# Performance work log

Hardware: AMD Instinct MI355X
Metric: run time of the kernel (lower is better)

## Reference

```python
import jax, jax.numpy as jnp
import numpy as np

D = 64
H = 256


def _directions(d):
    """Taylor-coefficient directions matching Bilaplacian._set_up_taylor_coefficients."""
    eye = np.eye(d, dtype=np.float32)
    dirs1 = 4.0 * eye                                   # (D, D): 4*e_i
    pairs_neq = np.array([(i, j) for i in range(d) for j in range(d) if i != j])
    dirs2 = 3.0 * eye[pairs_neq[:, 0]] + eye[pairs_neq[:, 1]]      # (D(D-1), D): 3 e_i + e_j
    pairs_lt = np.array([(i, j) for i in range(d) for j in range(i + 1, d)])
    dirs3 = 2.0 * eye[pairs_lt[:, 0]] + 2.0 * eye[pairs_lt[:, 1]]  # (D(D-1)/2, D): 2 e_i + 2 e_j
    return jnp.asarray(dirs1), jnp.asarray(dirs2), jnp.asarray(dirs3)


def setup_inputs() -> dict:
    key = jax.random.key(0)
    ks = jax.random.split(key, 7)
    x = jax.random.normal(ks[0], (D,), dtype=jnp.float32)
    W1 = jax.random.normal(ks[1], (H, D), dtype=jnp.float32) / np.sqrt(D)
    b1 = 0.1 * jax.random.normal(ks[2], (H,), dtype=jnp.float32)
    W2 = jax.random.normal(ks[3], (H, H), dtype=jnp.float32) / np.sqrt(H)
    b2 = 0.1 * jax.random.normal(ks[4], (H,), dtype=jnp.float32)
    W3 = jax.random.normal(ks[5], (1, H), dtype=jnp.float32) / np.sqrt(H)
    b3 = 0.1 * jax.random.normal(ks[6], (1,), dtype=jnp.float32)
    return {"x": x, "W1": W1, "b1": b1, "W2": W2, "b2": b2, "W3": W3, "b3": b3}


def _bilaplacian(x, W1, b1, W2, b2, W3, b3):
    d = x.shape[0]

    def f(z):
        h = jnp.tanh(W1 @ z + b1)
        h = jnp.tanh(W2 @ h + b2)
        return W3 @ h + b3  # (1,)

    def d4(v):
        # 4th directional derivative d^4/dt^4 f(x + t v) via Taylor-mode (nested jvp)
        g1 = lambda z: jax.jvp(f, (z,), (v,))[1]
        g2 = lambda z: jax.jvp(g1, (z,), (v,))[1]
        g3 = lambda z: jax.jvp(g2, (z,), (v,))[1]
        return jax.jvp(g3, (x,), (v,))[1]

    dirs1, dirs2, dirs3 = _directions(d)
    S1 = jax.vmap(d4)(dirs1).sum(0)
    S2 = jax.vmap(d4)(dirs2).sum(0)
    S3 = jax.vmap(d4)(dirs3).sum(0)
    # Polarization weights s.t. alpha*S1 + beta*S2 + gamma*S3 = sum_{i,j} d^4 f / dx_i^2 dx_j^2
    alpha = (1.0 + 13.0 * (d - 1) / 9.0) / 256.0
    beta = -1.0 / 36.0
    gamma = 5.0 / 96.0
    return alpha * S1 + beta * S2 + gamma * S3


def reference(x, W1, b1, W2, b2, W3, b3):
    return _bilaplacian(x, W1, b1, W2, b2, W3, b3)
```

## Files before the change

### kernel.cpp

```cpp
#include <hip/hip_runtime.h>
#include <hip/hip_bf16.h>


#define C_F    0
#define H0_F   1024
#define R2_F   1280
#define E_F    1536
#define Q_F    2560
#define S5_F   2816
#define U_F    3072
#define W1T_F  3328
#define G_F    19712
#define P_F    85248

__global__ __launch_bounds__(256) void k1_kernel(
    const float* __restrict__ x, const float* __restrict__ W1,
    const float* __restrict__ b1, float* __restrict__ ws_f,
    double* __restrict__ acc, int* __restrict__ cnt) {
    __shared__ __align__(16) float smem[2 * 64 * 68];
    int tid = threadIdx.x, b = blockIdx.x;

    if (b == 0) {
        float* xs = smem;
        if (tid < 64) xs[tid] = x[tid];
        __syncthreads();
        const float4* row = (const float4*)(W1 + tid * 64);
        const float4* xv4 = (const float4*)xs;
        float u0 = b1[tid], r2v = 0.f;
        #pragma unroll
        for (int k = 0; k < 16; k++) {
            float4 w = row[k], xv = xv4[k];
            u0  += w.x * xv.x + w.y * xv.y + w.z * xv.z + w.w * xv.w;
            r2v += w.x * w.x + w.y * w.y + w.z * w.z + w.w * w.w;
        }
        float T = tanhf(u0), s = 1.f - T * T;
        ws_f[C_F + tid]       = s;
        ws_f[C_F + 256 + tid] = -2.f * T * s;
        ws_f[C_F + 512 + tid] = s * (6.f * T * T - 2.f);
        ws_f[C_F + 768 + tid] = s * T * (16.f - 24.f * T * T);
        ws_f[H0_F + tid] = T;
        ws_f[R2_F + tid] = r2v;
        if (tid == 0) { *acc = 0.0; *cnt = 0; }
    } else if (b <= 16) {
        int tb = b - 1, nb = tb >> 2, pb = tb & 3;
        float* As = smem;
        float* Bs = smem + 64 * 68;
        for (int idx = tid; idx < 4096; idx += 256) {
            int r = idx >> 6, i = idx & 63;
            As[i * 68 + r] = W1[(nb * 64 + r) * 64 + i];
            Bs[i * 68 + r] = W1[(pb * 64 + r) * 64 + i];
        }
        __syncthreads();
        int r0 = (tid & 15) * 4, c0 = (tid >> 4) * 4;
        float a[4][4] = {};
        for (int i = 0; i < 64; i++) {
            float4 av = *(const float4*)&As[i * 68 + r0];
            float4 bv = *(const float4*)&Bs[i * 68 + c0];
            float ar[4] = {av.x, av.y, av.z, av.w};
            float br[4] = {bv.x, bv.y, bv.z, bv.w};
            #pragma unroll
            for (int rr = 0; rr < 4; rr++)
                #pragma unroll
                for (int cc = 0; cc < 4; cc++)
                    a[rr][cc] = fmaf(ar[rr], br[cc], a[rr][cc]);
        }
        float* G = ws_f + G_F;
        #pragma unroll
        for (int rr = 0; rr < 4; rr++)
            #pragma unroll
            for (int cc = 0; cc < 4; cc++)
                G[(nb * 64 + r0 + rr) * 256 + pb * 64 + c0 + cc] = a[rr][cc];
    } else {
        int base = (b - 17) * 4096;
        float* W1t = ws_f + W1T_F;
        for (int idx = base + tid; idx < base + 4096; idx += 256) {
            int n = idx >> 6, i = idx & 63;
            W1t[i * 256 + n] = W1[idx];
        }
    }
}

__global__ __launch_bounds__(256) void k2_kernel(
    const float* __restrict__ W1, const float* __restrict__ W2,
    const float* __restrict__ b2, const float* __restrict__ W3,
    float* __restrict__ ws_f) {
    __shared__ __align__(16) float smem[64 * 34 + 64 * 68];
    int tid = threadIdx.x, b = blockIdx.x;
    const float* c1g = ws_f + C_F;
    const float* c2g = ws_f + C_F + 256;
    const float* c4g = ws_f + C_F + 768;

    if (b < 8) {
        int m0 = b * 32;
        float* Wc = smem;
        float* Bc = smem + 64 * 34;
        float acc2[2][4] = {};
        int tm2 = (tid & 15) * 2, ti = (tid >> 4) * 4;
        for (int nc = 0; nc < 4; nc++) {
            __syncthreads();
            for (int idx = tid; idx < 2048; idx += 256) {
                int mm = idx >> 6, nn = idx & 63;
                Wc[nn * 34 + mm] = W2[(m0 + mm) * 256 + nc * 64 + nn];
            }
            for (int idx = tid; idx < 4096; idx += 256) {
                int nn = idx >> 6, ii = idx & 63, n = nc * 64 + nn;
                Bc[nn * 68 + ii] = c1g[n] * W1[n * 64 + ii];
            }
            __syncthreads();
            for (int nn = 0; nn < 64; nn++) {
                float2 a2 = *(const float2*)&Wc[nn * 34 + tm2];
                float4 b4 = *(const float4*)&Bc[nn * 68 + ti];
                float br[4] = {b4.x, b4.y, b4.z, b4.w};
                #pragma unroll
                for (int j = 0; j < 4; j++) {
                    acc2[0][j] = fmaf(a2.x, br[j], acc2[0][j]);
                    acc2[1][j] = fmaf(a2.y, br[j], acc2[1][j]);
                }
            }
        }
        float* P = ws_f + P_F;
        #pragma unroll
        for (int j = 0; j < 4; j++) {
            P[(m0 + tm2) * 64 + ti + j]     = acc2[0][j];
            P[(m0 + tm2 + 1) * 64 + ti + j] = acc2[1][j];
        }
    } else if (b < 12) {
        int m0 = (b - 8) * 64;
        float* Ws  = smem;
        float* h0s = smem + 64 * 65;
        float* part = h0s + 256;
        h0s[tid] = ws_f[H0_F + tid];
        int mm = tid & 63, nq = tid >> 6;
        float partial = 0.f;
        for (int nc = 0; nc < 4; nc++) {
            __syncthreads();
            for (int idx = tid; idx < 4096; idx += 256) {
                int m2 = idx >> 6, nn = idx & 63;
                Ws[nn * 65 + m2] = W2[(m0 + m2) * 256 + nc * 64 + nn];
            }
            __syncthreads();
            #pragma unroll
            for (int k = 0; k < 16; k++) {
                int nn = nq * 16 + k;
                partial = fmaf(Ws[nn * 65 + mm], h0s[nc * 64 + nn], partial);
            }
        }
        part[nq * 64 + mm] = partial;
        __syncthreads();
        if (tid < 64) {
            int m = m0 + tid;
            float v = b2[m] + part[tid] + part[64 + tid] + part[128 + tid] + part[192 + tid];
            float T2 = tanhf(v), s2 = 1.f - T2 * T2, w3 = W3[m];
            float* E = ws_f + E_F;
            E[m]       = w3 * s2;
            E[256 + m] = -2.f * w3 * T2 * s2;
            E[512 + m] = w3 * s2 * (6.f * T2 * T2 - 2.f);
            E[768 + m] = w3 * s2 * T2 * (16.f - 24.f * T2 * T2);
        }
    } else {
        int m = b - 12;
        float* cw  = smem;
        float* red = smem + 256;
        float w2r = W2[m * 256 + tid], c2r = c2g[tid];
        float cwv = c2r * w2r;
        cw[tid] = cwv;
        __syncthreads();
        const float* G = ws_f + G_F;
        float km = 0.f;
        #pragma unroll 4
        for (int np = 0; np < 256; np++) {
            float g = G[np * 256 + tid];
            km = fmaf(g * g, cw[np], km);
        }
        float r2r = ws_f[R2_F + tid], c4r = c4g[tid];
        float uv  = km * cwv;
        float qv  = cwv * r2r;
        float s5v = w2r * c4r * r2r * r2r;
        for (int o = 32; o > 0; o >>= 1) {
            uv  += __shfl_down(uv, o, 64);
            qv  += __shfl_down(qv, o, 64);
            s5v += __shfl_down(s5v, o, 64);
        }
        int w = tid >> 6;
        if ((tid & 63) == 0) { red[w * 3] = uv; red[w * 3 + 1] = qv; red[w * 3 + 2] = s5v; }
        __syncthreads();
        if (tid == 0) {
            ws_f[U_F + m]  = red[0] + red[3] + red[6] + red[9];
            ws_f[Q_F + m]  = red[1] + red[4] + red[7] + red[10];
            ws_f[S5_F + m] = red[2] + red[5] + red[8] + red[11];
        }
    }
}

__global__ __launch_bounds__(256) void k3_kernel(
    const float* __restrict__ W2, float* __restrict__ ws_f,
    double* __restrict__ acc, int* __restrict__ cnt, float* __restrict__ out) {
    __shared__ __align__(16) float smem[64 + 16];
    int tid = threadIdx.x, m = blockIdx.x;
    float* Ps  = smem;
    float* red = smem + 64;
    const float* P = ws_f + P_F;
    if (tid < 64) Ps[tid] = P[m * 64 + tid];
    __syncthreads();
    const float* W1t = ws_f + W1T_F;
    float T = 0.f;
    #pragma unroll 4
    for (int i = 0; i < 64; i++) T = fmaf(Ps[i], W1t[i * 256 + tid], T);
    float w2r = W2[m * 256 + tid];
    float c2r = ws_f[C_F + 256 + tid], c3r = ws_f[C_F + 512 + tid];
    float r2r = ws_f[R2_F + tid];
    float s3v = c2r * w2r * T * T;
    float s4v = c3r * r2r * w2r * T;
    float p2v = (tid < 64) ? Ps[tid] * Ps[tid] : 0.f;
    for (int o = 32; o > 0; o >>= 1) {
        s3v += __shfl_down(s3v, o, 64);
        s4v += __shfl_down(s4v, o, 64);
        p2v += __shfl_down(p2v, o, 64);
    }
    int w = tid >> 6;
    if ((tid & 63) == 0) { red[w * 3] = s3v; red[w * 3 + 1] = s4v; red[w * 3 + 2] = p2v; }
    __syncthreads();
    if (tid == 0) {
        float s3 = red[0] + red[3] + red[6] + red[9];
        float s4 = red[1] + red[4] + red[7] + red[10];
        float p2 = red[2] + red[5] + red[8] + red[11];
        const float* E = ws_f + E_F;
        float qm = ws_f[Q_F + m], um = ws_f[U_F + m], s5m = ws_f[S5_F + m];
        float y = E[768 + m] * p2 * p2
                + E[512 + m] * (2.f * qm * p2 + 4.f * s3)
                + E[256 + m] * (qm * qm + 2.f * um + 4.f * s4)
                + E[m] * s5m;
        atomicAdd(acc, (double)y);
        __threadfence();
        int t = atomicAdd(cnt, 1);
        if (t == 255) {
            __threadfence();
            out[0] = (float)atomicAdd(acc, 0.0);
        }
    }
}

extern "C" void kernel_launch(void* const* d_in, const int* in_sizes, int n_in,
                              void* d_out, int out_size, void* d_ws, size_t ws_size,
                              hipStream_t stream) {
    const float* x  = (const float*)d_in[0];
    const float* W1 = (const float*)d_in[1];
    const float* b1 = (const float*)d_in[2];
    const float* W2 = (const float*)d_in[3];
    const float* b2 = (const float*)d_in[4];
    const float* W3 = (const float*)d_in[5];

    char* ws = (char*)d_ws;
    double* acc  = (double*)ws;
    int*    cnt  = (int*)(ws + 8);
    float*  ws_f = (float*)(ws + 16);
    float*  out  = (float*)d_out;

    k1_kernel<<<21, 256, 0, stream>>>(x, W1, b1, ws_f, acc, cnt);
    k2_kernel<<<268, 256, 0, stream>>>(W1, W2, b2, W3, ws_f);
    k3_kernel<<<256, 256, 0, stream>>>(W2, ws_f, acc, cnt, out);
}
```

Baseline: 109.3 us.

## Recast per-row GEMV stages as tiled GEMMs with fused reductions and fewer blocks

The per-output-row blocks in k2 (the U term) and k3 (the S3/S4 terms) are replaced by 64x64 shared-memory tiled GEMMs with register blocking. Partial sums are reduced with shuffles and float atomics, and the Q, S5 and P2 reductions move into earlier blocks. The W1 transpose pass and the double-precision atomic accumulation are removed, and a last-block pattern does the final reduction. This cuts redundant global reads of G and W1t and the launch work, but leaves only 28 and 16 blocks, which may underuse the GPU, and makes the float atomic sums order-dependent.

Measured after the change: 104.6 us. -4.3%, faster.

```diff
diff --git a/kernel.cpp b/kernel.cpp
--- a/kernel.cpp
+++ b/kernel.cpp
@@ -9,14 +9,15 @@
 #define Q_F    2560
 #define S5_F   2816
 #define U_F    3072
-#define W1T_F  3328
-#define G_F    19712
-#define P_F    85248
+#define S3_F   3328
+#define S4_F   3584
+#define P2_F   3840
+#define G_F    4096
+#define P_F    69632
 
 __global__ __launch_bounds__(256) void k1_kernel(
     const float* __restrict__ x, const float* __restrict__ W1,
-    const float* __restrict__ b1, float* __restrict__ ws_f,
-    double* __restrict__ acc, int* __restrict__ cnt) {
+    const float* __restrict__ b1, float* __restrict__ ws_f, int* __restrict__ cnt) {
     __shared__ __align__(16) float smem[2 * 64 * 68];
     int tid = threadIdx.x, b = blockIdx.x;
 
@@ -40,8 +41,11 @@
         ws_f[C_F + 768 + tid] = s * T * (16.f - 24.f * T * T);
         ws_f[H0_F + tid] = T;
         ws_f[R2_F + tid] = r2v;
-        if (tid == 0) { *acc = 0.0; *cnt = 0; }
-    } else if (b <= 16) {
+        ws_f[U_F  + tid] = 0.f;
+        ws_f[S3_F + tid] = 0.f;
+        ws_f[S4_F + tid] = 0.f;
+        if (tid == 0) *cnt = 0;
+    } else {
         int tb = b - 1, nb = tb >> 2, pb = tb & 3;
         float* As = smem;
         float* Bs = smem + 64 * 68;
@@ -70,13 +74,6 @@
             #pragma unroll
             for (int cc = 0; cc < 4; cc++)
                 G[(nb * 64 + r0 + rr) * 256 + pb * 64 + c0 + cc] = a[rr][cc];
-    } else {
-        int base = (b - 17) * 4096;
-        float* W1t = ws_f + W1T_F;
-        for (int idx = base + tid; idx < base + 4096; idx += 256) {
-            int n = idx >> 6, i = idx & 63;
-            W1t[i * 256 + n] = W1[idx];
-        }
     }
 }
 
@@ -84,7 +81,7 @@
     const float* __restrict__ W1, const float* __restrict__ W2,
     const float* __restrict__ b2, const float* __restrict__ W3,
     float* __restrict__ ws_f) {
-    __shared__ __align__(16) float smem[64 * 34 + 64 * 68];
+    __shared__ __align__(16) float smem[13248];
     int tid = threadIdx.x, b = blockIdx.x;
     const float* c1g = ws_f + C_F;
     const float* c2g = ws_f + C_F + 256;
@@ -119,19 +116,38 @@
             }
         }
         float* P = ws_f + P_F;
+        float s0 = 0.f, s1 = 0.f;
         #pragma unroll
         for (int j = 0; j < 4; j++) {
             P[(m0 + tm2) * 64 + ti + j]     = acc2[0][j];
             P[(m0 + tm2 + 1) * 64 + ti + j] = acc2[1][j];
+            s0 += acc2[0][j] * acc2[0][j];
+            s1 += acc2[1][j] * acc2[1][j];
+        }
+        __syncthreads();
+        float* red = smem;
+        red[tm2 * 16 + (tid >> 4)]       = s0;
+        red[(tm2 + 1) * 16 + (tid >> 4)] = s1;
+        __syncthreads();
+        if (tid < 32) {
+            float p = 0.f;
+            #pragma unroll
+            for (int g = 0; g < 16; g++) p += red[tid * 16 + g];
+            ws_f[P2_F + m0 + tid] = p;
         }
     } else if (b < 12) {
         int m0 = (b - 8) * 64;
-        float* Ws  = smem;
-        float* h0s = smem + 64 * 65;
-        float* part = h0s + 256;
+        float* Ws   = smem;
+        float* h0s  = smem + 4160;
+        float* aqs  = h0s + 256;
+        float* a5s  = aqs + 256;
+        float* part = a5s + 256;
+        float r2v = ws_f[R2_F + tid];
         h0s[tid] = ws_f[H0_F + tid];
+        aqs[tid] = c2g[tid] * r2v;
+        a5s[tid] = c4g[tid] * r2v * r2v;
         int mm = tid & 63, nq = tid >> 6;
-        float partial = 0.f;
+        float pv = 0.f, pq = 0.f, p5 = 0.f;
         for (int nc = 0; nc < 4; nc++) {
             __syncthreads();
             for (int idx = tid; idx < 4096; idx += 256) {
@@ -141,102 +157,160 @@
             __syncthreads();
             #pragma unroll
             for (int k = 0; k < 16; k++) {
-                int nn = nq * 16 + k;
-                partial = fmaf(Ws[nn * 65 + mm], h0s[nc * 64 + nn], partial);
-            }
-        }
-        part[nq * 64 + mm] = partial;
+                int nn = nq * 16 + k, n = nc * 64 + nn;
+                float wv = Ws[nn * 65 + mm];
+                pv = fmaf(wv, h0s[n], pv);
+                pq = fmaf(wv, aqs[n], pq);
+                p5 = fmaf(wv, a5s[n], p5);
+            }
+        }
+        part[nq * 64 + mm]       = pv;
+        part[256 + nq * 64 + mm] = pq;
+        part[512 + nq * 64 + mm] = p5;
         __syncthreads();
         if (tid < 64) {
             int m = m0 + tid;
-            float v = b2[m] + part[tid] + part[64 + tid] + part[128 + tid] + part[192 + tid];
+            float v  = b2[m] + part[tid] + part[64 + tid] + part[128 + tid] + part[192 + tid];
+            float q  = part[256 + tid] + part[320 + tid] + part[384 + tid] + part[448 + tid];
+            float s5 = part[512 + tid] + part[576 + tid] + part[640 + tid] + part[704 + tid];
             float T2 = tanhf(v), s2 = 1.f - T2 * T2, w3 = W3[m];
             float* E = ws_f + E_F;
             E[m]       = w3 * s2;
             E[256 + m] = -2.f * w3 * T2 * s2;
             E[512 + m] = w3 * s2 * (6.f * T2 * T2 - 2.f);
             E[768 + m] = w3 * s2 * T2 * (16.f - 24.f * T2 * T2);
+            ws_f[Q_F + m]  = q;
+            ws_f[S5_F + m] = s5;
         }
     } else {
-        int m = b - 12;
-        float* cw  = smem;
-        float* red = smem + 256;
-        float w2r = W2[m * 256 + tid], c2r = c2g[tid];
-        float cwv = c2r * w2r;
-        cw[tid] = cwv;
-        __syncthreads();
+        int tb = b - 12, kb = tb >> 2, mb = tb & 3;
+        float* As  = smem;
+        float* Bs  = smem + 4352;
+        float* W2k = smem + 8704;
+        float* c2k = smem + 13056;
+        for (int idx = tid; idx < 4096; idx += 256) {
+            int a_ = idx >> 6, b_ = idx & 63;
+            W2k[a_ * 68 + b_] = W2[(mb * 64 + a_) * 256 + kb * 64 + b_];
+        }
+        if (tid < 64) c2k[tid] = c2g[kb * 64 + tid];
+        int r0 = (tid & 15) * 4, c0 = (tid >> 4) * 4;
+        float a[4][4] = {};
         const float* G = ws_f + G_F;
-        float km = 0.f;
-        #pragma unroll 4
-        for (int np = 0; np < 256; np++) {
-            float g = G[np * 256 + tid];
-            km = fmaf(g * g, cw[np], km);
-        }
-        float r2r = ws_f[R2_F + tid], c4r = c4g[tid];
-        float uv  = km * cwv;
-        float qv  = cwv * r2r;
-        float s5v = w2r * c4r * r2r * r2r;
-        for (int o = 32; o > 0; o >>= 1) {
-            uv  += __shfl_down(uv, o, 64);
-            qv  += __shfl_down(qv, o, 64);
-            s5v += __shfl_down(s5v, o, 64);
-        }
-        int w = tid >> 6;
-        if ((tid & 63) == 0) { red[w * 3] = uv; red[w * 3 + 1] = qv; red[w * 3 + 2] = s5v; }
-        __syncthreads();
-        if (tid == 0) {
-            ws_f[U_F + m]  = red[0] + red[3] + red[6] + red[9];
-            ws_f[Q_F + m]  = red[1] + red[4] + red[7] + red[10];
-            ws_f[S5_F + m] = red[2] + red[5] + red[8] + red[11];
+        for (int nc = 0; nc < 4; nc++) {
+            __syncthreads();
+            float c2v = c2g[nc * 64 + (tid & 63)];
+            for (int idx = tid; idx < 4096; idx += 256) {
+                int a_ = idx >> 6, b_ = idx & 63;
+                float gv = G[(kb * 64 + a_) * 256 + nc * 64 + b_];
+                As[b_ * 68 + a_] = c2v * gv * gv;
+                Bs[b_ * 68 + a_] = W2[(mb * 64 + a_) * 256 + nc * 64 + b_];
+            }
+            __syncthreads();
+            for (int nn = 0; nn < 64; nn++) {
+                float4 av = *(const float4*)&As[nn * 68 + r0];
+                float4 bv = *(const float4*)&Bs[nn * 68 + c0];
+                float ar[4] = {av.x, av.y, av.z, av.w};
+                float br[4] = {bv.x, bv.y, bv.z, bv.w};
+                #pragma unroll
+                for (int rr = 0; rr < 4; rr++)
+                    #pragma unroll
+                    for (int cc = 0; cc < 4; cc++)
+                        a[rr][cc] = fmaf(ar[rr], br[cc], a[rr][cc]);
+            }
+        }
+        #pragma unroll
+        for (int cc = 0; cc < 4; cc++) {
+            float up = 0.f;
+            #pragma unroll
+            for (int rr = 0; rr < 4; rr++)
+                up += a[rr][cc] * c2k[r0 + rr] * W2k[(c0 + cc) * 68 + r0 + rr];
+            up += __shfl_xor(up, 8, 16);
+            up += __shfl_xor(up, 4, 16);
+            up += __shfl_xor(up, 2, 16);
+            up += __shfl_xor(up, 1, 16);
+            if ((tid & 15) == 0)
+                atomicAdd(&ws_f[U_F + mb * 64 + c0 + cc], up);
         }
     }
 }
 
 __global__ __launch_bounds__(256) void k3_kernel(
-    const float* __restrict__ W2, float* __restrict__ ws_f,
-    double* __restrict__ acc, int* __restrict__ cnt, float* __restrict__ out) {
-    __shared__ __align__(16) float smem[64 + 16];
-    int tid = threadIdx.x, m = blockIdx.x;
-    float* Ps  = smem;
-    float* red = smem + 64;
+    const float* __restrict__ W1, const float* __restrict__ W2,
+    float* __restrict__ ws_f, int* __restrict__ cnt, float* __restrict__ out) {
+    __shared__ __align__(16) float smem[13248];
+    __shared__ int isLast;
+    __shared__ double dsum[4];
+    int tid = threadIdx.x, b = blockIdx.x;
+    int mb = b >> 2, nb = b & 3;
+    float* As  = smem;
+    float* Bs  = smem + 4352;
+    float* W2s = smem + 8704;
+    float* c2s = smem + 13056;
+    float* c34 = smem + 13120;
     const float* P = ws_f + P_F;
-    if (tid < 64) Ps[tid] = P[m * 64 + tid];
+    for (int idx = tid; idx < 4096; idx += 256) {
+        int a_ = idx >> 6, b_ = idx & 63;
+        As[b_ * 68 + a_]  = P[(mb * 64 + a_) * 64 + b_];
+        Bs[b_ * 68 + a_]  = W1[(nb * 64 + a_) * 64 + b_];
+        W2s[a_ * 68 + b_] = W2[(mb * 64 + a_) * 256 + nb * 64 + b_];
+    }
+    if (tid < 64) {
+        int n = nb * 64 + tid;
+        c2s[tid] = ws_f[C_F + 256 + n];
+        c34[tid] = ws_f[C_F + 512 + n] * ws_f[R2_F + n];
+    }
     __syncthreads();
-    const float* W1t = ws_f + W1T_F;
-    float T = 0.f;
-    #pragma unroll 4
-    for (int i = 0; i < 64; i++) T = fmaf(Ps[i], W1t[i * 256 + tid], T);
-    float w2r = W2[m * 256 + tid];
-    float c2r = ws_f[C_F + 256 + tid], c3r = ws_f[C_F + 512 + tid];
-    float r2r = ws_f[R2_F + tid];
-    float s3v = c2r * w2r * T * T;
-    float s4v = c3r * r2r * w2r * T;
-    float p2v = (tid < 64) ? Ps[tid] * Ps[tid] : 0.f;
-    for (int o = 32; o > 0; o >>= 1) {
-        s3v += __shfl_down(s3v, o, 64);
-        s4v += __shfl_down(s4v, o, 64);
-        p2v += __shfl_down(p2v, o, 64);
-    }
-    int w = tid >> 6;
-    if ((tid & 63) == 0) { red[w * 3] = s3v; red[w * 3 + 1] = s4v; red[w * 3 + 2] = p2v; }
+    int m0t = (tid >> 4) * 4, n0t = (tid & 15) * 4;
+    float a[4][4] = {};
+    for (int ii = 0; ii < 64; ii++) {
+        float4 av = *(const float4*)&As[ii * 68 + m0t];
+        float4 bv = *(const float4*)&Bs[ii * 68 + n0t];
+        float ar[4] = {av.x, av.y, av.z, av.w};
+        float br[4] = {bv.x, bv.y, bv.z, bv.w};
+        #pragma unroll
+        for (int rr = 0; rr < 4; rr++)
+            #pragma unroll
+            for (int cc = 0; cc < 4; cc++)
+                a[rr][cc] = fmaf(ar[rr], br[cc], a[rr][cc]);
+    }
+    #pragma unroll
+    for (int rr = 0; rr < 4; rr++) {
+        float s3p = 0.f, s4p = 0.f;
+        #pragma unroll
+        for (int cc = 0; cc < 4; cc++) {
+            float wv = W2s[(m0t + rr) * 68 + n0t + cc];
+            float t  = a[rr][cc];
+            s3p = fmaf(c2s[n0t + cc] * wv, t * t, s3p);
+            s4p = fmaf(c34[n0t + cc] * wv, t, s4p);
+        }
+        s3p += __shfl_xor(s3p, 8, 16); s4p += __shfl_xor(s4p, 8, 16);
+        s3p += __shfl_xor(s3p, 4, 16); s4p += __shfl_xor(s4p, 4, 16);
+        s3p += __shfl_xor(s3p, 2, 16); s4p += __shfl_xor(s4p, 2, 16);
+        s3p += __shfl_xor(s3p, 1, 16); s4p += __shfl_xor(s4p, 1, 16);
+        if ((tid & 15) == 0) {
+            atomicAdd(&ws_f[S3_F + mb * 64 + m0t + rr], s3p);
+            atomicAdd(&ws_f[S4_F + mb * 64 + m0t + rr], s4p);
+        }
+    }
+    __threadfence();
+    if (tid == 0) isLast = (atomicAdd(cnt, 1) == 15) ? 1 : 0;
     __syncthreads();
-    if (tid == 0) {
-        float s3 = red[0] + red[3] + red[6] + red[9];
-        float s4 = red[1] + red[4] + red[7] + red[10];
-        float p2 = red[2] + red[5] + red[8] + red[11];
+    if (isLast) {
+        int m = tid;
+        float s3m = atomicAdd(&ws_f[S3_F + m], 0.f);
+        float s4m = atomicAdd(&ws_f[S4_F + m], 0.f);
+        float p2 = ws_f[P2_F + m], q = ws_f[Q_F + m];
+        float um = ws_f[U_F + m],  s5 = ws_f[S5_F + m];
         const float* E = ws_f + E_F;
-        float qm = ws_f[Q_F + m], um = ws_f[U_F + m], s5m = ws_f[S5_F + m];
         float y = E[768 + m] * p2 * p2
-                + E[512 + m] * (2.f * qm * p2 + 4.f * s3)
-                + E[256 + m] * (qm * qm + 2.f * um + 4.f * s4)
-                + E[m] * s5m;
-        atomicAdd(acc, (double)y);
-        __threadfence();
-        int t = atomicAdd(cnt, 1);
-        if (t == 255) {
-            __threadfence();
-            out[0] = (float)atomicAdd(acc, 0.0);
-        }
+                + E[512 + m] * (2.f * q * p2 + 4.f * s3m)
+                + E[256 + m] * (q * q + 2.f * um + 4.f * s4m)
+                + E[m] * s5;
+        double part = (double)y;
+        for (int off = 32; off > 0; off >>= 1) part += __shfl_down(part, off, 64);
+        if ((tid & 63) == 0) dsum[tid >> 6] = part;
+        __syncthreads();
+        if (tid == 0) out[0] = (float)(dsum[0] + dsum[1] + dsum[2] + dsum[3]);
     }
 }
 
@@ -251,12 +325,11 @@
     const float* W3 = (const float*)d_in[5];
 
     char* ws = (char*)d_ws;
-    double* acc  = (double*)ws;
-    int*    cnt  = (int*)(ws + 8);
+    int*    cnt  = (int*)ws;
     float*  ws_f = (float*)(ws + 16);
     float*  out  = (float*)d_out;
 
-    k1_kernel<<<21, 256, 0, stream>>>(x, W1, b1, ws_f, acc, cnt);
-    k2_kernel<<<268, 256, 0, stream>>>(W1, W2, b2, W3, ws_f);
-    k3_kernel<<<256, 256, 0, stream>>>(W2, ws_f, acc, cnt, out);
+    k1_kernel<<<17, 256, 0, stream>>>(x, W1, b1, ws_f, cnt);
+    k2_kernel<<<28, 256, 0, stream>>>(W1, W2, b2, W3, ws_f);
+    k3_kernel<<<16, 256, 0, stream>>>(W1, W2, ws_f, cnt, out);
 }
```
